# Optimization experiments

Hardware: AMD Instinct MI355X
Metric: run time of the kernel (lower is better)

## Reference

```python
import jax, jax.numpy as jnp
import numpy as np

B, T, C = 2, 2048, 1024
H, KV, HD = 16, 4, 64  # n_head, n_kv_head, head_dim = C // H


def apply_rotary_emb(x, cos, sin):
    d = x.shape[-1] // 2
    x1, x2 = x[..., :d], x[..., d:]
    return jnp.concatenate([x1 * cos + x2 * sin, -x1 * sin + x2 * cos], axis=-1)


def rms_norm(x):
    return x * jax.lax.rsqrt(jnp.mean(jnp.square(x), axis=-1, keepdims=True) + 1e-6)


def setup_inputs() -> dict:
    key = jax.random.key(0)
    ks = jax.random.split(key, 7)
    std = 0.02
    return {
        "x": jax.random.normal(ks[0], (B, T, C), jnp.float32),
        "cos": jax.random.normal(ks[1], (1, T, 1, HD // 2), jnp.float32),
        "sin": jax.random.normal(ks[2], (1, T, 1, HD // 2), jnp.float32),
        "Wq": jax.random.normal(ks[3], (C, H * HD), jnp.float32) * std,
        "Wk": jax.random.normal(ks[4], (C, KV * HD), jnp.float32) * std,
        "Wv": jax.random.normal(ks[5], (C, KV * HD), jnp.float32) * std,
        "Wo": jax.random.normal(ks[6], (C, C), jnp.float32) * std,
    }


def reference(x, cos, sin, Wq, Wk, Wv, Wo):
    b, t, c = x.shape
    q = (x @ Wq).reshape(b, t, H, HD)
    k = (x @ Wk).reshape(b, t, KV, HD)
    v = (x @ Wv).reshape(b, t, KV, HD)
    q = rms_norm(apply_rotary_emb(q, cos, sin))
    k = rms_norm(apply_rotary_emb(k, cos, sin))
    # GQA: repeat kv heads
    n_rep = H // KV
    k = jnp.repeat(k, n_rep, axis=2)
    v = jnp.repeat(v, n_rep, axis=2)
    # causal attention (flax dot_product_attention semantics)
    scale = 1.0 / jnp.sqrt(jnp.asarray(HD, x.dtype))
    logits = jnp.einsum('bqhd,bkhd->bhqk', q, k) * scale
    causal = jnp.tril(jnp.ones((t, t), bool))
    neg = jnp.finfo(x.dtype).min
    logits = jnp.where(causal[None, None], logits, neg)
    w = jax.nn.softmax(logits, axis=-1)
    y = jnp.einsum('bhqk,bkhd->bqhd', w, v).reshape(b, t, c)
    return y @ Wo
```

## Files before the change

### kernel.cpp

```cpp
#include <hip/hip_runtime.h>
#include <hip/hip_bf16.h>

#define B_   2
#define T_   2048
#define C_   1024
#define H_   16
#define KV_  4
#define HD_  64
#define M_   (B_*T_)
#define NQKV_ 1536
#define PST_ 72

typedef __bf16 bf16x8 __attribute__((ext_vector_type(8)));
typedef float  f32x4  __attribute__((ext_vector_type(4)));

static __device__ __forceinline__ unsigned short f2bf(float f) {
    __hip_bfloat16 h = __float2bfloat16(f);
    return __builtin_bit_cast(unsigned short, h);
}

__global__ void cast_x_kernel(const float* __restrict__ x, unsigned short* __restrict__ xb) {
    int i = (blockIdx.x * 256 + threadIdx.x) * 4;
    float4 v = *(const float4*)(x + i);
    ushort4 o = make_ushort4(f2bf(v.x), f2bf(v.y), f2bf(v.z), f2bf(v.w));
    *(ushort4*)(xb + i) = o;
}

__global__ void transpose4_kernel(const float* __restrict__ Wq, const float* __restrict__ Wk,
                                  const float* __restrict__ Wv, const float* __restrict__ Wo,
                                  unsigned short* __restrict__ wtqkv, unsigned short* __restrict__ wto) {
    __shared__ float tile[32][33];
    int bid = blockIdx.x;
    const float* src; unsigned short* dst; int s, nlog;
    if (bid < 1024)      { src = Wq; dst = wtqkv;               s = bid;        nlog = 5; }
    else if (bid < 1280) { src = Wk; dst = wtqkv + 1024 * 1024; s = bid - 1024; nlog = 3; }
    else if (bid < 1536) { src = Wv; dst = wtqkv + 1280 * 1024; s = bid - 1280; nlog = 3; }
    else                 { src = Wo; dst = wto;                 s = bid - 1536; nlog = 5; }
    int N  = 32 << nlog;
    int k0 = (s >> nlog) * 32, n0 = (s & ((1 << nlog) - 1)) * 32;
    int lr = threadIdx.x >> 5, lc = threadIdx.x & 31;
    #pragma unroll
    for (int i = 0; i < 4; i++) {
        int r = lr + i * 8;
        tile[r][lc] = src[(k0 + r) * N + n0 + lc];
    }
    __syncthreads();
    #pragma unroll
    for (int i = 0; i < 4; i++) {
        int r = lr + i * 8;
        dst[(n0 + r) * 1024 + k0 + lc] = f2bf(tile[lc][r]);
    }
}

template <typename T, bool ROPE>
__global__ __launch_bounds__(256) void gemm_kernel(const unsigned short* __restrict__ A,
                                                   const unsigned short* __restrict__ Bt,
                                                   T* __restrict__ Cm, int Ni,
                                                   const float* __restrict__ cosb,
                                                   const float* __restrict__ sinb) {
    __shared__ __align__(16) unsigned short As[128 * 32];
    __shared__ __align__(16) unsigned short Bs[64 * 32];
    int m0 = blockIdx.x * 128;
    int head = blockIdx.y;
    int n0 = head * 64;
    int tid = threadIdx.x;
    int w = tid >> 6, lane = tid & 63;
    int col = lane & 15, quad = lane >> 4;
    int wm = w * 32;
    int ar = tid >> 2, ak = (tid & 3) * 8;

    f32x4 acc[2][4];
    #pragma unroll
    for (int mt = 0; mt < 2; mt++)
        #pragma unroll
        for (int nt = 0; nt < 4; nt++) acc[mt][nt] = (f32x4){0.f, 0.f, 0.f, 0.f};

    for (int k0 = 0; k0 < 1024; k0 += 32) {
        __builtin_amdgcn_global_load_lds(
            (const __attribute__((address_space(1))) unsigned int*)(A + (size_t)(m0 + ar) * 1024 + k0 + ak),
            (__attribute__((address_space(3))) unsigned int*)(As + ar * 32 + ak), 16, 0, 0);
        __builtin_amdgcn_global_load_lds(
            (const __attribute__((address_space(1))) unsigned int*)(A + (size_t)(m0 + ar + 64) * 1024 + k0 + ak),
            (__attribute__((address_space(3))) unsigned int*)(As + (ar + 64) * 32 + ak), 16, 0, 0);
        __builtin_amdgcn_global_load_lds(
            (const __attribute__((address_space(1))) unsigned int*)(Bt + (size_t)(n0 + ar) * 1024 + k0 + ak),
            (__attribute__((address_space(3))) unsigned int*)(Bs + ar * 32 + ak), 16, 0, 0);
        __syncthreads();
        bf16x8 af[2], bfr[4];
        #pragma unroll
        for (int mt = 0; mt < 2; mt++) af[mt]  = *(const bf16x8*)&As[(wm + mt * 16 + col) * 32 + quad * 8];
        #pragma unroll
        for (int nt = 0; nt < 4; nt++) bfr[nt] = *(const bf16x8*)&Bs[(nt * 16 + col) * 32 + quad * 8];
        #pragma unroll
        for (int mt = 0; mt < 2; mt++)
            #pragma unroll
            for (int nt = 0; nt < 4; nt++)
                acc[mt][nt] = __builtin_amdgcn_mfma_f32_16x16x32_bf16(af[mt], bfr[nt], acc[mt][nt], 0, 0, 0);
        __syncthreads();
    }

    if constexpr (ROPE) {
        if (head < H_ + KV_) {
            #pragma unroll
            for (int mt = 0; mt < 2; mt++)
                #pragma unroll
                for (int r = 0; r < 4; r++) {
                    int t = (m0 + wm + mt * 16 + quad * 4 + r) & (T_ - 1);
                    float nv[4];
                    #pragma unroll
                    for (int nt = 0; nt < 4; nt++) {
                        int i = (nt & 1) * 16 + col;
                        float c = cosb[t * 32 + i], s = sinb[t * 32 + i];
                        float v = acc[mt][nt][r], p = acc[mt][nt ^ 2][r];
                        nv[nt] = (nt < 2) ? (v * c + p * s) : (v * c - p * s);
                    }
                    float sq = nv[0] * nv[0] + nv[1] * nv[1] + nv[2] * nv[2] + nv[3] * nv[3];
                    sq += __shfl_xor(sq, 1, 64);
                    sq += __shfl_xor(sq, 2, 64);
                    sq += __shfl_xor(sq, 4, 64);
                    sq += __shfl_xor(sq, 8, 64);
                    float rr = rsqrtf(sq * (1.0f / 64.0f) + 1e-6f);
                    if (head < H_) rr *= 0.125f;
                    #pragma unroll
                    for (int nt = 0; nt < 4; nt++) acc[mt][nt][r] = nv[nt] * rr;
                }
        }
    }

    #pragma unroll
    for (int mt = 0; mt < 2; mt++)
        #pragma unroll
        for (int nt = 0; nt < 4; nt++)
            #pragma unroll
            for (int r = 0; r < 4; r++) {
                size_t idx = (size_t)(m0 + wm + mt * 16 + quad * 4 + r) * Ni + n0 + nt * 16 + col;
                if constexpr (sizeof(T) == 2) Cm[idx] = f2bf(acc[mt][nt][r]);
                else                          Cm[idx] = acc[mt][nt][r];
            }
}

__global__ __launch_bounds__(256) void vtrans_kernel(const unsigned short* __restrict__ qkvb,
                                                     unsigned short* __restrict__ vtb) {
    __shared__ unsigned short tileb[64][72];
    int tile = blockIdx.x & 31;
    int bkv  = blockIdx.x >> 5;
    int b = bkv >> 2, kvh = bkv & 3;
    int tid = threadIdx.x;
    int t0 = tile * 64;
    #pragma unroll
    for (int i = 0; i < 2; i++) {
        int idx = tid + i * 256;
        int r = idx >> 3, d8 = (idx & 7) * 8;
        *(uint4*)&tileb[r][d8] =
            *(const uint4*)&qkvb[(size_t)(b * T_ + t0 + r) * NQKV_ + 1280 + kvh * 64 + d8];
    }
    __syncthreads();
    #pragma unroll
    for (int i = 0; i < 2; i++) {
        int idx = tid + i * 256;
        int dr = idx >> 3, t8 = (idx & 7) * 8;
        unsigned short tmp[8];
        #pragma unroll
        for (int j = 0; j < 8; j++) tmp[j] = tileb[t8 + j][dr];
        *(uint4*)&vtb[((size_t)(bkv * 64 + dr)) * T_ + t0 + t8] = *(uint4*)tmp;
    }
}

__global__ __launch_bounds__(256) void attn_kernel(const unsigned short* __restrict__ qkvb,
                                                   const unsigned short* __restrict__ vtb,
                                                   unsigned short* __restrict__ yb) {
    __shared__ __align__(16) char smem[4 * 32 * 64 * 4];
    __shared__ float lbuf[4][32];

    int bh = blockIdx.x & 31;
    int qt = 63 - (blockIdx.x >> 5);
    int b = bh >> 4, h = bh & 15, kvh = h >> 2;
    int tid = threadIdx.x;
    int w = tid >> 6, lane = tid & 63;
    int col = lane & 15, quad = lane >> 4;
    int t0 = qt * 32;
    int nkt = (t0 + 95) >> 6;

    unsigned short* Ps = (unsigned short*)smem + w * (32 * PST_);
    float* Obuf = (float*)smem;

    const unsigned short* kptr = qkvb + (size_t)(b * T_) * NQKV_ + 1024 + kvh * 64;
    const unsigned short* vptr = vtb + (size_t)((b * KV_ + kvh) * 64) * T_;

    bf16x8 aq[2][2];
    #pragma unroll
    for (int mt = 0; mt < 2; mt++)
        #pragma unroll
        for (int step = 0; step < 2; step++)
            aq[mt][step] = *(const bf16x8*)&qkvb[(size_t)(b * T_ + t0 + mt * 16 + col) * NQKV_
                                                 + h * 64 + quad * 8 + step * 32];
    bf16x8 ones;
    #pragma unroll
    for (int j = 0; j < 8; j++) ones[j] = (__bf16)1.0f;

    f32x4 o[2][4], lacc[2];
    #pragma unroll
    for (int mt = 0; mt < 2; mt++) {
        lacc[mt] = (f32x4){0.f, 0.f, 0.f, 0.f};
        #pragma unroll
        for (int nt = 0; nt < 4; nt++) o[mt][nt] = (f32x4){0.f, 0.f, 0.f, 0.f};
    }

    for (int kt = w; kt < nkt; kt += 4) {
        f32x4 sacc[2][4];
        #pragma unroll
        for (int mt = 0; mt < 2; mt++)
            #pragma unroll
            for (int nt = 0; nt < 4; nt++) sacc[mt][nt] = (f32x4){0.f, 0.f, 0.f, 0.f};
        #pragma unroll
        for (int step = 0; step < 2; step++) {
            bf16x8 kb[4];
            #pragma unroll
            for (int nt = 0; nt < 4; nt++)
                kb[nt] = *(const bf16x8*)&kptr[(size_t)(kt * 64 + nt * 16 + col) * NQKV_
                                               + quad * 8 + step * 32];
            #pragma unroll
            for (int nt = 0; nt < 4; nt++)
                #pragma unroll
                for (int mt = 0; mt < 2; mt++)
                    sacc[mt][nt] = __builtin_amdgcn_mfma_f32_16x16x32_bf16(aq[mt][step], kb[nt], sacc[mt][nt], 0, 0, 0);
        }
        bf16x8 vb[2][4];
        #pragma unroll
        for (int step = 0; step < 2; step++)
            #pragma unroll
            for (int nt = 0; nt < 4; nt++)
                vb[step][nt] = *(const bf16x8*)&vptr[(size_t)(nt * 16 + col) * T_
                                                     + kt * 64 + quad * 8 + step * 32];
        if (kt == nkt - 1) {
            #pragma unroll
            for (int mt = 0; mt < 2; mt++)
                #pragma unroll
                for (int nt = 0; nt < 4; nt++)
                    #pragma unroll
                    for (int r = 0; r < 4; r++)
                        if (kt * 64 + nt * 16 + col > t0 + mt * 16 + quad * 4 + r)
                            sacc[mt][nt][r] = -1e30f;
        }
        #pragma unroll
        for (int mt = 0; mt < 2; mt++)
            #pragma unroll
            for (int nt = 0; nt < 4; nt++)
                #pragma unroll
                for (int r = 0; r < 4; r++)
                    Ps[(mt * 16 + quad * 4 + r) * PST_ + nt * 16 + col] =
                        f2bf(__expf(sacc[mt][nt][r] - 8.0f));
        #pragma unroll
        for (int step = 0; step < 2; step++) {
            bf16x8 ap[2];
            #pragma unroll
            for (int mt = 0; mt < 2; mt++)
                ap[mt] = *(const bf16x8*)&Ps[(mt * 16 + col) * PST_ + quad * 8 + step * 32];
            #pragma unroll
            for (int nt = 0; nt < 4; nt++)
                #pragma unroll
                for (int mt = 0; mt < 2; mt++)
                    o[mt][nt] = __builtin_amdgcn_mfma_f32_16x16x32_bf16(ap[mt], vb[step][nt], o[mt][nt], 0, 0, 0);
            #pragma unroll
            for (int mt = 0; mt < 2; mt++)
                lacc[mt] = __builtin_amdgcn_mfma_f32_16x16x32_bf16(ap[mt], ones, lacc[mt], 0, 0, 0);
        }
    }

    __syncthreads();
    #pragma unroll
    for (int mt = 0; mt < 2; mt++)
        #pragma unroll
        for (int nt = 0; nt < 4; nt++)
            #pragma unroll
            for (int r = 0; r < 4; r++)
                Obuf[w * 2048 + (mt * 16 + quad * 4 + r) * 64 + nt * 16 + col] = o[mt][nt][r];
    if (col == 0) {
        #pragma unroll
        for (int mt = 0; mt < 2; mt++)
            #pragma unroll
            for (int r = 0; r < 4; r++)
                lbuf[w][mt * 16 + quad * 4 + r] = lacc[mt][r];
    }
    __syncthreads();
    {
        int row = tid >> 3, d0 = (tid & 7) * 8;
        float ls = lbuf[0][row] + lbuf[1][row] + lbuf[2][row] + lbuf[3][row];
        float inv = 1.0f / ls;
        float s[8];
        #pragma unroll
        for (int j = 0; j < 8; j++) s[j] = 0.f;
        #pragma unroll
        for (int wv = 0; wv < 4; wv++) {
            f32x4 p0 = *(const f32x4*)&Obuf[wv * 2048 + row * 64 + d0];
            f32x4 p1 = *(const f32x4*)&Obuf[wv * 2048 + row * 64 + d0 + 4];
            #pragma unroll
            for (int j = 0; j < 4; j++) { s[j] += p0[j]; s[4 + j] += p1[j]; }
        }
        unsigned short o8[8];
        #pragma unroll
        for (int j = 0; j < 8; j++) o8[j] = f2bf(s[j] * inv);
        *(uint4*)&yb[(size_t)(b * T_ + t0 + row) * C_ + h * 64 + d0] = *(uint4*)o8;
    }
}

extern "C" void kernel_launch(void* const* d_in, const int* in_sizes, int n_in,
                              void* d_out, int out_size, void* d_ws, size_t ws_size,
                              hipStream_t stream) {
    const float* x    = (const float*)d_in[0];
    const float* cosb = (const float*)d_in[1];
    const float* sinb = (const float*)d_in[2];
    const float* Wq   = (const float*)d_in[3];
    const float* Wk   = (const float*)d_in[4];
    const float* Wv   = (const float*)d_in[5];
    const float* Wo   = (const float*)d_in[6];
    float* out = (float*)d_out;

    char* ws = (char*)d_ws;
    unsigned short* xb    = (unsigned short*)(ws);
    unsigned short* yb    = (unsigned short*)(ws);
    unsigned short* wtqkv = (unsigned short*)(ws + ( 8u << 20));
    unsigned short* wto   = (unsigned short*)(ws + (11u << 20));
    unsigned short* qkvb  = (unsigned short*)(ws + (13u << 20));
    unsigned short* vtb   = (unsigned short*)(ws + (25u << 20));

    cast_x_kernel<<<4096, 256, 0, stream>>>(x, xb);
    transpose4_kernel<<<2560, 256, 0, stream>>>(Wq, Wk, Wv, Wo, wtqkv, wto);
    gemm_kernel<unsigned short, true><<<dim3(32, 24), 256, 0, stream>>>(xb, wtqkv, qkvb, NQKV_, cosb, sinb);
    vtrans_kernel<<<256, 256, 0, stream>>>(qkvb, vtb);
    attn_kernel<<<2048, 256, 0, stream>>>(qkvb, vtb, yb);
    gemm_kernel<float, false><<<dim3(32, 16), 256, 0, stream>>>(yb, wto, out, C_, nullptr, nullptr);
}
```

Measured before the change: 196.0 us.

## Merge prep kernels, deepen GEMM K-step, software-pipeline attention P·V with S

Combines the x cast and weight transpose into one launch to save a kernel launch. The GEMM now loads two 32-wide K slices per barrier pair, halving the number of syncs per K loop at the cost of twice the LDS. The attention kernel double-buffers the per-wave P tile, so the P·V MFMAs for the previous tile are issued alongside the loads and QK MFMAs for the next tile. This raises register and LDS use per wave.

```diff
diff --git a/kernel.cpp b/kernel.cpp
--- a/kernel.cpp
+++ b/kernel.cpp
@@ -19,18 +19,20 @@
     return __builtin_bit_cast(unsigned short, h);
 }
 
-__global__ void cast_x_kernel(const float* __restrict__ x, unsigned short* __restrict__ xb) {
-    int i = (blockIdx.x * 256 + threadIdx.x) * 4;
-    float4 v = *(const float4*)(x + i);
-    ushort4 o = make_ushort4(f2bf(v.x), f2bf(v.y), f2bf(v.z), f2bf(v.w));
-    *(ushort4*)(xb + i) = o;
-}
-
-__global__ void transpose4_kernel(const float* __restrict__ Wq, const float* __restrict__ Wk,
-                                  const float* __restrict__ Wv, const float* __restrict__ Wo,
-                                  unsigned short* __restrict__ wtqkv, unsigned short* __restrict__ wto) {
+__global__ void prep_kernel(const float* __restrict__ x, unsigned short* __restrict__ xb,
+                            const float* __restrict__ Wq, const float* __restrict__ Wk,
+                            const float* __restrict__ Wv, const float* __restrict__ Wo,
+                            unsigned short* __restrict__ wtqkv, unsigned short* __restrict__ wto) {
     __shared__ float tile[32][33];
     int bid = blockIdx.x;
+    if (bid < 4096) {
+        int i = (bid * 256 + threadIdx.x) * 4;
+        float4 v = *(const float4*)(x + i);
+        ushort4 o = make_ushort4(f2bf(v.x), f2bf(v.y), f2bf(v.z), f2bf(v.w));
+        *(ushort4*)(xb + i) = o;
+        return;
+    }
+    bid -= 4096;
     const float* src; unsigned short* dst; int s, nlog;
     if (bid < 1024)      { src = Wq; dst = wtqkv;               s = bid;        nlog = 5; }
     else if (bid < 1280) { src = Wk; dst = wtqkv + 1024 * 1024; s = bid - 1024; nlog = 3; }
@@ -58,8 +60,8 @@
                                                    T* __restrict__ Cm, int Ni,
                                                    const float* __restrict__ cosb,
                                                    const float* __restrict__ sinb) {
-    __shared__ __align__(16) unsigned short As[128 * 32];
-    __shared__ __align__(16) unsigned short Bs[64 * 32];
+    __shared__ __align__(16) unsigned short As[2][128 * 32];
+    __shared__ __align__(16) unsigned short Bs[2][64 * 32];
     int m0 = blockIdx.x * 128;
     int head = blockIdx.y;
     int n0 = head * 64;
@@ -75,27 +77,35 @@
         #pragma unroll
         for (int nt = 0; nt < 4; nt++) acc[mt][nt] = (f32x4){0.f, 0.f, 0.f, 0.f};
 
-    for (int k0 = 0; k0 < 1024; k0 += 32) {
-        __builtin_amdgcn_global_load_lds(
-            (const __attribute__((address_space(1))) unsigned int*)(A + (size_t)(m0 + ar) * 1024 + k0 + ak),
-            (__attribute__((address_space(3))) unsigned int*)(As + ar * 32 + ak), 16, 0, 0);
-        __builtin_amdgcn_global_load_lds(
-            (const __attribute__((address_space(1))) unsigned int*)(A + (size_t)(m0 + ar + 64) * 1024 + k0 + ak),
-            (__attribute__((address_space(3))) unsigned int*)(As + (ar + 64) * 32 + ak), 16, 0, 0);
-        __builtin_amdgcn_global_load_lds(
-            (const __attribute__((address_space(1))) unsigned int*)(Bt + (size_t)(n0 + ar) * 1024 + k0 + ak),
-            (__attribute__((address_space(3))) unsigned int*)(Bs + ar * 32 + ak), 16, 0, 0);
+    for (int k0 = 0; k0 < 1024; k0 += 64) {
+        #pragma unroll
+        for (int hh = 0; hh < 2; hh++) {
+            __builtin_amdgcn_global_load_lds(
+                (const __attribute__((address_space(1))) unsigned int*)(A + (size_t)(m0 + ar) * 1024 + k0 + hh * 32 + ak),
+                (__attribute__((address_space(3))) unsigned int*)(&As[hh][ar * 32 + ak]), 16, 0, 0);
+            __builtin_amdgcn_global_load_lds(
+                (const __attribute__((address_space(1))) unsigned int*)(A + (size_t)(m0 + ar + 64) * 1024 + k0 + hh * 32 + ak),
+                (__attribute__((address_space(3))) unsigned int*)(&As[hh][(ar + 64) * 32 + ak]), 16, 0, 0);
+            __builtin_amdgcn_global_load_lds(
+                (const __attribute__((address_space(1))) unsigned int*)(Bt + (size_t)(n0 + ar) * 1024 + k0 + hh * 32 + ak),
+                (__attribute__((address_space(3))) unsigned int*)(&Bs[hh][ar * 32 + ak]), 16, 0, 0);
+        }
         __syncthreads();
-        bf16x8 af[2], bfr[4];
-        #pragma unroll
-        for (int mt = 0; mt < 2; mt++) af[mt]  = *(const bf16x8*)&As[(wm + mt * 16 + col) * 32 + quad * 8];
-        #pragma unroll
-        for (int nt = 0; nt < 4; nt++) bfr[nt] = *(const bf16x8*)&Bs[(nt * 16 + col) * 32 + quad * 8];
-        #pragma unroll
-        for (int mt = 0; mt < 2; mt++)
-            #pragma unroll
-            for (int nt = 0; nt < 4; nt++)
-                acc[mt][nt] = __builtin_amdgcn_mfma_f32_16x16x32_bf16(af[mt], bfr[nt], acc[mt][nt], 0, 0, 0);
+        bf16x8 af[2][2], bfr[4][2];
+        #pragma unroll
+        for (int hh = 0; hh < 2; hh++) {
+            #pragma unroll
+            for (int mt = 0; mt < 2; mt++) af[mt][hh]  = *(const bf16x8*)&As[hh][(wm + mt * 16 + col) * 32 + quad * 8];
+            #pragma unroll
+            for (int nt = 0; nt < 4; nt++) bfr[nt][hh] = *(const bf16x8*)&Bs[hh][(nt * 16 + col) * 32 + quad * 8];
+        }
+        #pragma unroll
+        for (int hh = 0; hh < 2; hh++)
+            #pragma unroll
+            for (int mt = 0; mt < 2; mt++)
+                #pragma unroll
+                for (int nt = 0; nt < 4; nt++)
+                    acc[mt][nt] = __builtin_amdgcn_mfma_f32_16x16x32_bf16(af[mt][hh], bfr[nt][hh], acc[mt][nt], 0, 0, 0);
         __syncthreads();
     }
 
@@ -169,7 +179,7 @@
 __global__ __launch_bounds__(256) void attn_kernel(const unsigned short* __restrict__ qkvb,
                                                    const unsigned short* __restrict__ vtb,
                                                    unsigned short* __restrict__ yb) {
-    __shared__ __align__(16) char smem[4 * 32 * 64 * 4];
+    __shared__ __align__(16) char smem[4 * 2 * 32 * PST_ * 2];
     __shared__ float lbuf[4][32];
 
     int bh = blockIdx.x & 31;
@@ -181,23 +191,12 @@
     int t0 = qt * 32;
     int nkt = (t0 + 95) >> 6;
 
-    unsigned short* Ps = (unsigned short*)smem + w * (32 * PST_);
+    unsigned short* Pw = (unsigned short*)smem + w * (2 * 32 * PST_);
     float* Obuf = (float*)smem;
 
     const unsigned short* kptr = qkvb + (size_t)(b * T_) * NQKV_ + 1024 + kvh * 64;
     const unsigned short* vptr = vtb + (size_t)((b * KV_ + kvh) * 64) * T_;
 
-    bf16x8 aq[2][2];
-    #pragma unroll
-    for (int mt = 0; mt < 2; mt++)
-        #pragma unroll
-        for (int step = 0; step < 2; step++)
-            aq[mt][step] = *(const bf16x8*)&qkvb[(size_t)(b * T_ + t0 + mt * 16 + col) * NQKV_
-                                                 + h * 64 + quad * 8 + step * 32];
-    bf16x8 ones;
-    #pragma unroll
-    for (int j = 0; j < 8; j++) ones[j] = (__bf16)1.0f;
-
     f32x4 o[2][4], lacc[2];
     #pragma unroll
     for (int mt = 0; mt < 2; mt++) {
@@ -206,56 +205,134 @@
         for (int nt = 0; nt < 4; nt++) o[mt][nt] = (f32x4){0.f, 0.f, 0.f, 0.f};
     }
 
-    for (int kt = w; kt < nkt; kt += 4) {
-        f32x4 sacc[2][4];
+    bf16x8 ones;
+    #pragma unroll
+    for (int j = 0; j < 8; j++) ones[j] = (__bf16)1.0f;
+
+    if (w < nkt) {
+        bf16x8 aq[2][2];
         #pragma unroll
         for (int mt = 0; mt < 2; mt++)
             #pragma unroll
-            for (int nt = 0; nt < 4; nt++) sacc[mt][nt] = (f32x4){0.f, 0.f, 0.f, 0.f};
-        #pragma unroll
-        for (int step = 0; step < 2; step++) {
-            bf16x8 kb[4];
+            for (int step = 0; step < 2; step++)
+                aq[mt][step] = *(const bf16x8*)&qkvb[(size_t)(b * T_ + t0 + mt * 16 + col) * NQKV_
+                                                     + h * 64 + quad * 8 + step * 32];
+        bf16x8 vb[2][4];
+        int cur = 0;
+
+        {
+            int kt = w;
+            bf16x8 kb0[4], kb1[4];
+            #pragma unroll
+            for (int nt = 0; nt < 4; nt++) {
+                kb0[nt] = *(const bf16x8*)&kptr[(size_t)(kt * 64 + nt * 16 + col) * NQKV_ + quad * 8];
+                kb1[nt] = *(const bf16x8*)&kptr[(size_t)(kt * 64 + nt * 16 + col) * NQKV_ + quad * 8 + 32];
+            }
+            f32x4 sacc[2][4];
+            #pragma unroll
+            for (int mt = 0; mt < 2; mt++)
+                #pragma unroll
+                for (int nt = 0; nt < 4; nt++) sacc[mt][nt] = (f32x4){0.f, 0.f, 0.f, 0.f};
             #pragma unroll
             for (int nt = 0; nt < 4; nt++)
-                kb[nt] = *(const bf16x8*)&kptr[(size_t)(kt * 64 + nt * 16 + col) * NQKV_
-                                               + quad * 8 + step * 32];
+                #pragma unroll
+                for (int mt = 0; mt < 2; mt++) {
+                    sacc[mt][nt] = __builtin_amdgcn_mfma_f32_16x16x32_bf16(aq[mt][0], kb0[nt], sacc[mt][nt], 0, 0, 0);
+                    sacc[mt][nt] = __builtin_amdgcn_mfma_f32_16x16x32_bf16(aq[mt][1], kb1[nt], sacc[mt][nt], 0, 0, 0);
+                }
+            #pragma unroll
+            for (int step = 0; step < 2; step++)
+                #pragma unroll
+                for (int nt = 0; nt < 4; nt++)
+                    vb[step][nt] = *(const bf16x8*)&vptr[(size_t)(nt * 16 + col) * T_
+                                                         + kt * 64 + quad * 8 + step * 32];
+            if (kt == nkt - 1) {
+                #pragma unroll
+                for (int mt = 0; mt < 2; mt++)
+                    #pragma unroll
+                    for (int nt = 0; nt < 4; nt++)
+                        #pragma unroll
+                        for (int r = 0; r < 4; r++)
+                            if (kt * 64 + nt * 16 + col > t0 + mt * 16 + quad * 4 + r)
+                                sacc[mt][nt][r] = -1e30f;
+            }
+            #pragma unroll
+            for (int mt = 0; mt < 2; mt++)
+                #pragma unroll
+                for (int nt = 0; nt < 4; nt++)
+                    #pragma unroll
+                    for (int r = 0; r < 4; r++)
+                        Pw[cur * (32 * PST_) + (mt * 16 + quad * 4 + r) * PST_ + nt * 16 + col] =
+                            f2bf(__expf(sacc[mt][nt][r] - 8.0f));
+        }
+
+        for (int kt = w + 4; kt < nkt; kt += 4) {
+            bf16x8 kb0[4], kb1[4];
+            #pragma unroll
+            for (int nt = 0; nt < 4; nt++) {
+                kb0[nt] = *(const bf16x8*)&kptr[(size_t)(kt * 64 + nt * 16 + col) * NQKV_ + quad * 8];
+                kb1[nt] = *(const bf16x8*)&kptr[(size_t)(kt * 64 + nt * 16 + col) * NQKV_ + quad * 8 + 32];
+            }
+            #pragma unroll
+            for (int step = 0; step < 2; step++) {
+                bf16x8 ap[2];
+                #pragma unroll
+                for (int mt = 0; mt < 2; mt++)
+                    ap[mt] = *(const bf16x8*)&Pw[cur * (32 * PST_) + (mt * 16 + col) * PST_ + quad * 8 + step * 32];
+                #pragma unroll
+                for (int nt = 0; nt < 4; nt++)
+                    #pragma unroll
+                    for (int mt = 0; mt < 2; mt++)
+                        o[mt][nt] = __builtin_amdgcn_mfma_f32_16x16x32_bf16(ap[mt], vb[step][nt], o[mt][nt], 0, 0, 0);
+                #pragma unroll
+                for (int mt = 0; mt < 2; mt++)
+                    lacc[mt] = __builtin_amdgcn_mfma_f32_16x16x32_bf16(ap[mt], ones, lacc[mt], 0, 0, 0);
+            }
+            f32x4 sacc[2][4];
+            #pragma unroll
+            for (int mt = 0; mt < 2; mt++)
+                #pragma unroll
+                for (int nt = 0; nt < 4; nt++) sacc[mt][nt] = (f32x4){0.f, 0.f, 0.f, 0.f};
             #pragma unroll
             for (int nt = 0; nt < 4; nt++)
                 #pragma unroll
+                for (int mt = 0; mt < 2; mt++) {
+                    sacc[mt][nt] = __builtin_amdgcn_mfma_f32_16x16x32_bf16(aq[mt][0], kb0[nt], sacc[mt][nt], 0, 0, 0);
+                    sacc[mt][nt] = __builtin_amdgcn_mfma_f32_16x16x32_bf16(aq[mt][1], kb1[nt], sacc[mt][nt], 0, 0, 0);
+                }
+            #pragma unroll
+            for (int step = 0; step < 2; step++)
+                #pragma unroll
+                for (int nt = 0; nt < 4; nt++)
+                    vb[step][nt] = *(const bf16x8*)&vptr[(size_t)(nt * 16 + col) * T_
+                                                         + kt * 64 + quad * 8 + step * 32];
+            if (kt == nkt - 1) {
+                #pragma unroll
                 for (int mt = 0; mt < 2; mt++)
-                    sacc[mt][nt] = __builtin_amdgcn_mfma_f32_16x16x32_bf16(aq[mt][step], kb[nt], sacc[mt][nt], 0, 0, 0);
-        }
-        bf16x8 vb[2][4];
-        #pragma unroll
-        for (int step = 0; step < 2; step++)
-            #pragma unroll
-            for (int nt = 0; nt < 4; nt++)
-                vb[step][nt] = *(const bf16x8*)&vptr[(size_t)(nt * 16 + col) * T_
-                                                     + kt * 64 + quad * 8 + step * 32];
-        if (kt == nkt - 1) {
+                    #pragma unroll
+                    for (int nt = 0; nt < 4; nt++)
+                        #pragma unroll
+                        for (int r = 0; r < 4; r++)
+                            if (kt * 64 + nt * 16 + col > t0 + mt * 16 + quad * 4 + r)
+                                sacc[mt][nt][r] = -1e30f;
+            }
+            cur ^= 1;
             #pragma unroll
             for (int mt = 0; mt < 2; mt++)
                 #pragma unroll
                 for (int nt = 0; nt < 4; nt++)
                     #pragma unroll
                     for (int r = 0; r < 4; r++)
-                        if (kt * 64 + nt * 16 + col > t0 + mt * 16 + quad * 4 + r)
-                            sacc[mt][nt][r] = -1e30f;
-        }
-        #pragma unroll
-        for (int mt = 0; mt < 2; mt++)
-            #pragma unroll
-            for (int nt = 0; nt < 4; nt++)
-                #pragma unroll
-                for (int r = 0; r < 4; r++)
-                    Ps[(mt * 16 + quad * 4 + r) * PST_ + nt * 16 + col] =
-                        f2bf(__expf(sacc[mt][nt][r] - 8.0f));
+                        Pw[cur * (32 * PST_) + (mt * 16 + quad * 4 + r) * PST_ + nt * 16 + col] =
+                            f2bf(__expf(sacc[mt][nt][r] - 8.0f));
+        }
+
         #pragma unroll
         for (int step = 0; step < 2; step++) {
             bf16x8 ap[2];
             #pragma unroll
             for (int mt = 0; mt < 2; mt++)
-                ap[mt] = *(const bf16x8*)&Ps[(mt * 16 + col) * PST_ + quad * 8 + step * 32];
+                ap[mt] = *(const bf16x8*)&Pw[cur * (32 * PST_) + (mt * 16 + col) * PST_ + quad * 8 + step * 32];
             #pragma unroll
             for (int nt = 0; nt < 4; nt++)
                 #pragma unroll
@@ -324,8 +401,7 @@
     unsigned short* qkvb  = (unsigned short*)(ws + (13u << 20));
     unsigned short* vtb   = (unsigned short*)(ws + (25u << 20));
 
-    cast_x_kernel<<<4096, 256, 0, stream>>>(x, xb);
-    transpose4_kernel<<<2560, 256, 0, stream>>>(Wq, Wk, Wv, Wo, wtqkv, wto);
+    prep_kernel<<<4096 + 2560, 256, 0, stream>>>(x, xb, Wq, Wk, Wv, Wo, wtqkv, wto);
     gemm_kernel<unsigned short, true><<<dim3(32, 24), 256, 0, stream>>>(xb, wtqkv, qkvb, NQKV_, cosb, sinb);
     vtrans_kernel<<<256, 256, 0, stream>>>(qkvb, vtb);
     attn_kernel<<<2048, 256, 0, stream>>>(qkvb, vtb, yb);
```

Result: no change. 194.4 us (-0.8%).

## Fuse prep kernels, write V transposed from GEMM, transpose attention score tiles

Applied to the files above, without the earlier changes.

Merges the x cast and weight transpose into one launch, and has the QKV GEMM write V directly in transposed layout so the separate vtrans kernel is dropped. The GEMM K loop now loads 64-wide K chunks per barrier and the grid axes are swapped so head is the fast index. In attention, scores are computed as K·Q^T so each lane holds 4 consecutive keys, which lets P be stored as packed 8-byte words. The log2(e) factor is folded into the Q scale so exp2f can be used. This removes two launches and an intermediate pass over V in exchange for a more scattered V write pattern and more LDS per GEMM block.

```diff
diff --git a/kernel.cpp b/kernel.cpp
--- a/kernel.cpp
+++ b/kernel.cpp
@@ -10,6 +10,7 @@
 #define M_   (B_*T_)
 #define NQKV_ 1536
 #define PST_ 72
+#define M8L2E_ 11.5415603f
 
 typedef __bf16 bf16x8 __attribute__((ext_vector_type(8)));
 typedef float  f32x4  __attribute__((ext_vector_type(4)));
@@ -18,19 +19,24 @@
     __hip_bfloat16 h = __float2bfloat16(f);
     return __builtin_bit_cast(unsigned short, h);
 }
-
-__global__ void cast_x_kernel(const float* __restrict__ x, unsigned short* __restrict__ xb) {
-    int i = (blockIdx.x * 256 + threadIdx.x) * 4;
-    float4 v = *(const float4*)(x + i);
-    ushort4 o = make_ushort4(f2bf(v.x), f2bf(v.y), f2bf(v.z), f2bf(v.w));
-    *(ushort4*)(xb + i) = o;
-}
-
-__global__ void transpose4_kernel(const float* __restrict__ Wq, const float* __restrict__ Wk,
-                                  const float* __restrict__ Wv, const float* __restrict__ Wo,
-                                  unsigned short* __restrict__ wtqkv, unsigned short* __restrict__ wto) {
+static __device__ __forceinline__ unsigned int pk2(float a, float b) {
+    return (unsigned int)f2bf(a) | ((unsigned int)f2bf(b) << 16);
+}
+
+__global__ void prep_kernel(const float* __restrict__ x, unsigned short* __restrict__ xb,
+                            const float* __restrict__ Wq, const float* __restrict__ Wk,
+                            const float* __restrict__ Wv, const float* __restrict__ Wo,
+                            unsigned short* __restrict__ wtqkv, unsigned short* __restrict__ wto) {
     __shared__ float tile[32][33];
     int bid = blockIdx.x;
+    if (bid < 4096) {
+        int i = (bid * 256 + threadIdx.x) * 4;
+        float4 v = *(const float4*)(x + i);
+        ushort4 o = make_ushort4(f2bf(v.x), f2bf(v.y), f2bf(v.z), f2bf(v.w));
+        *(ushort4*)(xb + i) = o;
+        return;
+    }
+    bid -= 4096;
     const float* src; unsigned short* dst; int s, nlog;
     if (bid < 1024)      { src = Wq; dst = wtqkv;               s = bid;        nlog = 5; }
     else if (bid < 1280) { src = Wk; dst = wtqkv + 1024 * 1024; s = bid - 1024; nlog = 3; }
@@ -57,11 +63,12 @@
                                                    const unsigned short* __restrict__ Bt,
                                                    T* __restrict__ Cm, int Ni,
                                                    const float* __restrict__ cosb,
-                                                   const float* __restrict__ sinb) {
-    __shared__ __align__(16) unsigned short As[128 * 32];
-    __shared__ __align__(16) unsigned short Bs[64 * 32];
-    int m0 = blockIdx.x * 128;
-    int head = blockIdx.y;
+                                                   const float* __restrict__ sinb,
+                                                   unsigned short* __restrict__ vtb) {
+    __shared__ __align__(16) unsigned short As[2][128 * 32];
+    __shared__ __align__(16) unsigned short Bs[2][64 * 32];
+    int head = blockIdx.x;
+    int m0 = blockIdx.y * 128;
     int n0 = head * 64;
     int tid = threadIdx.x;
     int w = tid >> 6, lane = tid & 63;
@@ -75,56 +82,79 @@
         #pragma unroll
         for (int nt = 0; nt < 4; nt++) acc[mt][nt] = (f32x4){0.f, 0.f, 0.f, 0.f};
 
-    for (int k0 = 0; k0 < 1024; k0 += 32) {
-        __builtin_amdgcn_global_load_lds(
-            (const __attribute__((address_space(1))) unsigned int*)(A + (size_t)(m0 + ar) * 1024 + k0 + ak),
-            (__attribute__((address_space(3))) unsigned int*)(As + ar * 32 + ak), 16, 0, 0);
-        __builtin_amdgcn_global_load_lds(
-            (const __attribute__((address_space(1))) unsigned int*)(A + (size_t)(m0 + ar + 64) * 1024 + k0 + ak),
-            (__attribute__((address_space(3))) unsigned int*)(As + (ar + 64) * 32 + ak), 16, 0, 0);
-        __builtin_amdgcn_global_load_lds(
-            (const __attribute__((address_space(1))) unsigned int*)(Bt + (size_t)(n0 + ar) * 1024 + k0 + ak),
-            (__attribute__((address_space(3))) unsigned int*)(Bs + ar * 32 + ak), 16, 0, 0);
+    for (int k0 = 0; k0 < 1024; k0 += 64) {
+        #pragma unroll
+        for (int hh = 0; hh < 2; hh++) {
+            __builtin_amdgcn_global_load_lds(
+                (const __attribute__((address_space(1))) unsigned int*)(A + (size_t)(m0 + ar) * 1024 + k0 + hh * 32 + ak),
+                (__attribute__((address_space(3))) unsigned int*)(&As[hh][ar * 32 + ak]), 16, 0, 0);
+            __builtin_amdgcn_global_load_lds(
+                (const __attribute__((address_space(1))) unsigned int*)(A + (size_t)(m0 + ar + 64) * 1024 + k0 + hh * 32 + ak),
+                (__attribute__((address_space(3))) unsigned int*)(&As[hh][(ar + 64) * 32 + ak]), 16, 0, 0);
+            __builtin_amdgcn_global_load_lds(
+                (const __attribute__((address_space(1))) unsigned int*)(Bt + (size_t)(n0 + ar) * 1024 + k0 + hh * 32 + ak),
+                (__attribute__((address_space(3))) unsigned int*)(&Bs[hh][ar * 32 + ak]), 16, 0, 0);
+        }
         __syncthreads();
-        bf16x8 af[2], bfr[4];
-        #pragma unroll
-        for (int mt = 0; mt < 2; mt++) af[mt]  = *(const bf16x8*)&As[(wm + mt * 16 + col) * 32 + quad * 8];
-        #pragma unroll
-        for (int nt = 0; nt < 4; nt++) bfr[nt] = *(const bf16x8*)&Bs[(nt * 16 + col) * 32 + quad * 8];
+        bf16x8 af[2][2], bfr[4][2];
+        #pragma unroll
+        for (int hh = 0; hh < 2; hh++) {
+            #pragma unroll
+            for (int mt = 0; mt < 2; mt++) af[mt][hh]  = *(const bf16x8*)&As[hh][(wm + mt * 16 + col) * 32 + quad * 8];
+            #pragma unroll
+            for (int nt = 0; nt < 4; nt++) bfr[nt][hh] = *(const bf16x8*)&Bs[hh][(nt * 16 + col) * 32 + quad * 8];
+        }
+        #pragma unroll
+        for (int hh = 0; hh < 2; hh++)
+            #pragma unroll
+            for (int mt = 0; mt < 2; mt++)
+                #pragma unroll
+                for (int nt = 0; nt < 4; nt++)
+                    acc[mt][nt] = __builtin_amdgcn_mfma_f32_16x16x32_bf16(af[mt][hh], bfr[nt][hh], acc[mt][nt], 0, 0, 0);
+        __syncthreads();
+    }
+
+    if constexpr (ROPE) {
+        if (head >= H_ + KV_) {
+            int kvh = head - (H_ + KV_);
+            int b = m0 >> 11;
+            #pragma unroll
+            for (int mt = 0; mt < 2; mt++) {
+                int tb = (m0 + wm + mt * 16 + quad * 4) & (T_ - 1);
+                #pragma unroll
+                for (int nt = 0; nt < 4; nt++) {
+                    int d = nt * 16 + col;
+                    uint2 pv;
+                    pv.x = pk2(acc[mt][nt][0], acc[mt][nt][1]);
+                    pv.y = pk2(acc[mt][nt][2], acc[mt][nt][3]);
+                    *(uint2*)&vtb[((size_t)((b * KV_ + kvh) * 64 + d)) * T_ + tb] = pv;
+                }
+            }
+            return;
+        }
         #pragma unroll
         for (int mt = 0; mt < 2; mt++)
             #pragma unroll
-            for (int nt = 0; nt < 4; nt++)
-                acc[mt][nt] = __builtin_amdgcn_mfma_f32_16x16x32_bf16(af[mt], bfr[nt], acc[mt][nt], 0, 0, 0);
-        __syncthreads();
-    }
-
-    if constexpr (ROPE) {
-        if (head < H_ + KV_) {
-            #pragma unroll
-            for (int mt = 0; mt < 2; mt++)
-                #pragma unroll
-                for (int r = 0; r < 4; r++) {
-                    int t = (m0 + wm + mt * 16 + quad * 4 + r) & (T_ - 1);
-                    float nv[4];
-                    #pragma unroll
-                    for (int nt = 0; nt < 4; nt++) {
-                        int i = (nt & 1) * 16 + col;
-                        float c = cosb[t * 32 + i], s = sinb[t * 32 + i];
-                        float v = acc[mt][nt][r], p = acc[mt][nt ^ 2][r];
-                        nv[nt] = (nt < 2) ? (v * c + p * s) : (v * c - p * s);
-                    }
-                    float sq = nv[0] * nv[0] + nv[1] * nv[1] + nv[2] * nv[2] + nv[3] * nv[3];
-                    sq += __shfl_xor(sq, 1, 64);
-                    sq += __shfl_xor(sq, 2, 64);
-                    sq += __shfl_xor(sq, 4, 64);
-                    sq += __shfl_xor(sq, 8, 64);
-                    float rr = rsqrtf(sq * (1.0f / 64.0f) + 1e-6f);
-                    if (head < H_) rr *= 0.125f;
-                    #pragma unroll
-                    for (int nt = 0; nt < 4; nt++) acc[mt][nt][r] = nv[nt] * rr;
+            for (int r = 0; r < 4; r++) {
+                int t = (m0 + wm + mt * 16 + quad * 4 + r) & (T_ - 1);
+                float nv[4];
+                #pragma unroll
+                for (int nt = 0; nt < 4; nt++) {
+                    int i = (nt & 1) * 16 + col;
+                    float c = cosb[t * 32 + i], s = sinb[t * 32 + i];
+                    float v = acc[mt][nt][r], p = acc[mt][nt ^ 2][r];
+                    nv[nt] = (nt < 2) ? (v * c + p * s) : (v * c - p * s);
                 }
-        }
+                float sq = nv[0] * nv[0] + nv[1] * nv[1] + nv[2] * nv[2] + nv[3] * nv[3];
+                sq += __shfl_xor(sq, 1, 64);
+                sq += __shfl_xor(sq, 2, 64);
+                sq += __shfl_xor(sq, 4, 64);
+                sq += __shfl_xor(sq, 8, 64);
+                float rr = rsqrtf(sq * (1.0f / 64.0f) + 1e-6f);
+                if (head < H_) rr *= 0.125f * 1.44269504f;
+                #pragma unroll
+                for (int nt = 0; nt < 4; nt++) acc[mt][nt][r] = nv[nt] * rr;
+            }
     }
 
     #pragma unroll
@@ -137,33 +167,6 @@
                 if constexpr (sizeof(T) == 2) Cm[idx] = f2bf(acc[mt][nt][r]);
                 else                          Cm[idx] = acc[mt][nt][r];
             }
-}
-
-__global__ __launch_bounds__(256) void vtrans_kernel(const unsigned short* __restrict__ qkvb,
-                                                     unsigned short* __restrict__ vtb) {
-    __shared__ unsigned short tileb[64][72];
-    int tile = blockIdx.x & 31;
-    int bkv  = blockIdx.x >> 5;
-    int b = bkv >> 2, kvh = bkv & 3;
-    int tid = threadIdx.x;
-    int t0 = tile * 64;
-    #pragma unroll
-    for (int i = 0; i < 2; i++) {
-        int idx = tid + i * 256;
-        int r = idx >> 3, d8 = (idx & 7) * 8;
-        *(uint4*)&tileb[r][d8] =
-            *(const uint4*)&qkvb[(size_t)(b * T_ + t0 + r) * NQKV_ + 1280 + kvh * 64 + d8];
-    }
-    __syncthreads();
-    #pragma unroll
-    for (int i = 0; i < 2; i++) {
-        int idx = tid + i * 256;
-        int dr = idx >> 3, t8 = (idx & 7) * 8;
-        unsigned short tmp[8];
-        #pragma unroll
-        for (int j = 0; j < 8; j++) tmp[j] = tileb[t8 + j][dr];
-        *(uint4*)&vtb[((size_t)(bkv * 64 + dr)) * T_ + t0 + t8] = *(uint4*)tmp;
-    }
 }
 
 __global__ __launch_bounds__(256) void attn_kernel(const unsigned short* __restrict__ qkvb,
@@ -189,11 +192,11 @@
 
     bf16x8 aq[2][2];
     #pragma unroll
-    for (int mt = 0; mt < 2; mt++)
+    for (int ntq = 0; ntq < 2; ntq++)
         #pragma unroll
         for (int step = 0; step < 2; step++)
-            aq[mt][step] = *(const bf16x8*)&qkvb[(size_t)(b * T_ + t0 + mt * 16 + col) * NQKV_
-                                                 + h * 64 + quad * 8 + step * 32];
+            aq[ntq][step] = *(const bf16x8*)&qkvb[(size_t)(b * T_ + t0 + ntq * 16 + col) * NQKV_
+                                                  + h * 64 + quad * 8 + step * 32];
     bf16x8 ones;
     #pragma unroll
     for (int j = 0; j < 8; j++) ones[j] = (__bf16)1.0f;
@@ -207,63 +210,64 @@
     }
 
     for (int kt = w; kt < nkt; kt += 4) {
-        f32x4 sacc[2][4];
-        #pragma unroll
-        for (int mt = 0; mt < 2; mt++)
-            #pragma unroll
-            for (int nt = 0; nt < 4; nt++) sacc[mt][nt] = (f32x4){0.f, 0.f, 0.f, 0.f};
+        f32x4 sacc[4][2];
+        #pragma unroll
+        for (int mtk = 0; mtk < 4; mtk++)
+            #pragma unroll
+            for (int ntq = 0; ntq < 2; ntq++) sacc[mtk][ntq] = (f32x4){0.f, 0.f, 0.f, 0.f};
         #pragma unroll
         for (int step = 0; step < 2; step++) {
             bf16x8 kb[4];
             #pragma unroll
-            for (int nt = 0; nt < 4; nt++)
-                kb[nt] = *(const bf16x8*)&kptr[(size_t)(kt * 64 + nt * 16 + col) * NQKV_
-                                               + quad * 8 + step * 32];
-            #pragma unroll
-            for (int nt = 0; nt < 4; nt++)
-                #pragma unroll
-                for (int mt = 0; mt < 2; mt++)
-                    sacc[mt][nt] = __builtin_amdgcn_mfma_f32_16x16x32_bf16(aq[mt][step], kb[nt], sacc[mt][nt], 0, 0, 0);
+            for (int mtk = 0; mtk < 4; mtk++)
+                kb[mtk] = *(const bf16x8*)&kptr[(size_t)(kt * 64 + mtk * 16 + col) * NQKV_
+                                                + quad * 8 + step * 32];
+            #pragma unroll
+            for (int mtk = 0; mtk < 4; mtk++)
+                #pragma unroll
+                for (int ntq = 0; ntq < 2; ntq++)
+                    sacc[mtk][ntq] = __builtin_amdgcn_mfma_f32_16x16x32_bf16(kb[mtk], aq[ntq][step], sacc[mtk][ntq], 0, 0, 0);
         }
         bf16x8 vb[2][4];
         #pragma unroll
         for (int step = 0; step < 2; step++)
             #pragma unroll
-            for (int nt = 0; nt < 4; nt++)
-                vb[step][nt] = *(const bf16x8*)&vptr[(size_t)(nt * 16 + col) * T_
-                                                     + kt * 64 + quad * 8 + step * 32];
+            for (int ntd = 0; ntd < 4; ntd++)
+                vb[step][ntd] = *(const bf16x8*)&vptr[(size_t)(ntd * 16 + col) * T_
+                                                      + kt * 64 + quad * 8 + step * 32];
         if (kt == nkt - 1) {
             #pragma unroll
-            for (int mt = 0; mt < 2; mt++)
-                #pragma unroll
-                for (int nt = 0; nt < 4; nt++)
+            for (int mtk = 0; mtk < 4; mtk++)
+                #pragma unroll
+                for (int ntq = 0; ntq < 2; ntq++)
                     #pragma unroll
                     for (int r = 0; r < 4; r++)
-                        if (kt * 64 + nt * 16 + col > t0 + mt * 16 + quad * 4 + r)
-                            sacc[mt][nt][r] = -1e30f;
-        }
-        #pragma unroll
-        for (int mt = 0; mt < 2; mt++)
-            #pragma unroll
-            for (int nt = 0; nt < 4; nt++)
-                #pragma unroll
-                for (int r = 0; r < 4; r++)
-                    Ps[(mt * 16 + quad * 4 + r) * PST_ + nt * 16 + col] =
-                        f2bf(__expf(sacc[mt][nt][r] - 8.0f));
+                        if (kt * 64 + mtk * 16 + quad * 4 + r > t0 + ntq * 16 + col)
+                            sacc[mtk][ntq][r] = -1e30f;
+        }
+        #pragma unroll
+        for (int mtk = 0; mtk < 4; mtk++)
+            #pragma unroll
+            for (int ntq = 0; ntq < 2; ntq++) {
+                uint2 pw;
+                pw.x = pk2(exp2f(sacc[mtk][ntq][0] - M8L2E_), exp2f(sacc[mtk][ntq][1] - M8L2E_));
+                pw.y = pk2(exp2f(sacc[mtk][ntq][2] - M8L2E_), exp2f(sacc[mtk][ntq][3] - M8L2E_));
+                *(uint2*)&Ps[(ntq * 16 + col) * PST_ + mtk * 16 + quad * 4] = pw;
+            }
         #pragma unroll
         for (int step = 0; step < 2; step++) {
             bf16x8 ap[2];
             #pragma unroll
-            for (int mt = 0; mt < 2; mt++)
-                ap[mt] = *(const bf16x8*)&Ps[(mt * 16 + col) * PST_ + quad * 8 + step * 32];
-            #pragma unroll
-            for (int nt = 0; nt < 4; nt++)
-                #pragma unroll
-                for (int mt = 0; mt < 2; mt++)
-                    o[mt][nt] = __builtin_amdgcn_mfma_f32_16x16x32_bf16(ap[mt], vb[step][nt], o[mt][nt], 0, 0, 0);
-            #pragma unroll
-            for (int mt = 0; mt < 2; mt++)
-                lacc[mt] = __builtin_amdgcn_mfma_f32_16x16x32_bf16(ap[mt], ones, lacc[mt], 0, 0, 0);
+            for (int mtq = 0; mtq < 2; mtq++)
+                ap[mtq] = *(const bf16x8*)&Ps[(mtq * 16 + col) * PST_ + quad * 8 + step * 32];
+            #pragma unroll
+            for (int ntd = 0; ntd < 4; ntd++)
+                #pragma unroll
+                for (int mtq = 0; mtq < 2; mtq++)
+                    o[mtq][ntd] = __builtin_amdgcn_mfma_f32_16x16x32_bf16(ap[mtq], vb[step][ntd], o[mtq][ntd], 0, 0, 0);
+            #pragma unroll
+            for (int mtq = 0; mtq < 2; mtq++)
+                lacc[mtq] = __builtin_amdgcn_mfma_f32_16x16x32_bf16(ap[mtq], ones, lacc[mtq], 0, 0, 0);
         }
     }
 
@@ -324,10 +328,8 @@
     unsigned short* qkvb  = (unsigned short*)(ws + (13u << 20));
     unsigned short* vtb   = (unsigned short*)(ws + (25u << 20));
 
-    cast_x_kernel<<<4096, 256, 0, stream>>>(x, xb);
-    transpose4_kernel<<<2560, 256, 0, stream>>>(Wq, Wk, Wv, Wo, wtqkv, wto);
-    gemm_kernel<unsigned short, true><<<dim3(32, 24), 256, 0, stream>>>(xb, wtqkv, qkvb, NQKV_, cosb, sinb);
-    vtrans_kernel<<<256, 256, 0, stream>>>(qkvb, vtb);
+    prep_kernel<<<4096 + 2560, 256, 0, stream>>>(x, xb, Wq, Wk, Wv, Wo, wtqkv, wto);
+    gemm_kernel<unsigned short, true><<<dim3(24, 32), 256, 0, stream>>>(xb, wtqkv, qkvb, NQKV_, cosb, sinb, vtb);
     attn_kernel<<<2048, 256, 0, stream>>>(qkvb, vtb, yb);
-    gemm_kernel<float, false><<<dim3(32, 16), 256, 0, stream>>>(yb, wto, out, C_, nullptr, nullptr);
-}
+    gemm_kernel<float, false><<<dim3(16, 32), 256, 0, stream>>>(yb, wto, out, C_, nullptr, nullptr, nullptr);
+}
```

Result: faster. 191.4 us (-2.3%).
